# Kernel tuning notes

Measured on AMD Instinct MI355X. Metric: run time of the kernel, lower is better.

## Reference

```python
import jax, jax.numpy as jnp
import numpy as np

EMB = 512
HID = 1024
BATCH = 64
TX = 512


def setup_inputs() -> dict:
    key = jax.random.key(0)
    ks = jax.random.split(key, 9)
    s = 0.05
    return {
        "word": jax.random.normal(ks[0], (BATCH, TX, EMB), dtype=jnp.float32),
        "Wz": jax.random.normal(ks[1], (HID, HID + EMB), dtype=jnp.float32) * s,
        "bz": jax.random.normal(ks[2], (HID,), dtype=jnp.float32) * s,
        "Wr": jax.random.normal(ks[3], (HID, HID + EMB), dtype=jnp.float32) * s,
        "br": jax.random.normal(ks[4], (HID,), dtype=jnp.float32) * s,
        "Wh": jax.random.normal(ks[5], (HID, HID + EMB), dtype=jnp.float32) * s,
        "bh": jax.random.normal(ks[6], (HID,), dtype=jnp.float32) * s,
        "Wy": jax.random.normal(ks[7], (EMB, HID), dtype=jnp.float32) * s,
        "by": jax.random.normal(ks[8], (EMB,), dtype=jnp.float32) * s,
    }


def reference(word, Wz, bz, Wr, br, Wh, bh, Wy, by):
    batch = word.shape[0]
    word_t = jnp.transpose(word, (1, 0, 2))  # [T, B, E]
    h0 = jnp.zeros((batch, HID), dtype=word.dtype)
    x0 = jnp.zeros((batch, EMB), dtype=word.dtype)

    def step(carry, w_i):
        h, x = carry  # x is the PREVIOUS timestep's word (lags by one, as in the torch code)
        comb = jnp.concatenate([h, x], axis=1)  # [B, HID+EMB]
        z = jax.nn.sigmoid(comb @ Wz.T + bz)
        r = jax.nn.sigmoid(comb @ Wr.T + br)
        comb2 = jnp.concatenate([r * h, x], axis=1)
        h_tilde = jnp.tanh(comb2 @ Wh.T + bh)
        h_new = (1.0 - z) * h + z * h_tilde
        y = h_new @ Wy.T + by  # [B, E]
        return (h_new, w_i), y

    _, ys = jax.lax.scan(step, (h0, x0), word_t)  # ys: [T, B, E]
    return jnp.transpose(ys, (1, 0, 2))  # [B, T, E]
```

## Files before the change

### kernel.cpp

```cpp
#include <hip/hip_runtime.h>
#include <hip/hip_bf16.h>


#define EMB 512
#define HID 1024
#define BATCHN 64
#define TLEN 512
#define CAT 1536
#define GROUPS 4
#define GB 16
#define WPG 32
#define HX_LD 1024
#define ZL_LD 34
#define GPAD 8

typedef __attribute__((ext_vector_type(8))) short bf16x8;
typedef __attribute__((ext_vector_type(4))) short s16x4;
typedef __attribute__((ext_vector_type(4))) float f32x4;
typedef unsigned int u32;
typedef unsigned long long u64;
typedef unsigned short u16;

__device__ __forceinline__ float bf2f(u16 u) {
  union { float f; u32 i; } v; v.i = ((u32)u) << 16; return v.f;
}
__device__ __forceinline__ u16 f2bf(float f) {
  union { float f; u32 i; } v; v.f = f;
  u32 r = v.i + 0x7fffu + ((v.i >> 16) & 1u);
  return (u16)(r >> 16);
}

__device__ __forceinline__ u64 ld_dc(const u16* p) {
  return __hip_atomic_load((const u64*)p, __ATOMIC_RELAXED, __HIP_MEMORY_SCOPE_AGENT);
}
__device__ __forceinline__ void st_dc16(u16* p, u16 v) {
  __hip_atomic_store(p, v, __ATOMIC_RELAXED, __HIP_MEMORY_SCOPE_AGENT);
}

__global__ __launch_bounds__(256) void convert_gate_w(const float* __restrict__ W,
                                                      u16* __restrict__ Wh_,
                                                      u16* __restrict__ Wx_) {
  int i = blockIdx.x * 256 + threadIdx.x;
  if (i >= HID * CAT) return;
  int row = i / CAT, col = i - row * CAT;
  u16 v = f2bf(W[i]);
  if (col < HID) Wh_[row * HID + col] = v;
  else           Wx_[row * EMB + (col - HID)] = v;
}

__global__ __launch_bounds__(256) void convert_wy(const float* __restrict__ W, u16* __restrict__ Wy_) {
  int i = blockIdx.x * 256 + threadIdx.x;
  if (i < EMB * HID) Wy_[i] = f2bf(W[i]);
}

__global__ __launch_bounds__(256) void proj_kernel(const float* __restrict__ word,
                                                   const u16* __restrict__ Wx,
                                                   const float* __restrict__ bias,
                                                   u16* __restrict__ P) {
  __shared__ __align__(16) u16 As[64][64 + GPAD];
  __shared__ __align__(16) u16 Bs[64][64 + GPAD];
  const int tid = threadIdx.x;
  const int wid = tid >> 6, lane = tid & 63;
  const int m0 = blockIdx.x * 64, n0 = blockIdx.y * 64;
  const int mw = (wid >> 1) * 32, nw = (wid & 1) * 32;
  f32x4 acc[2][2] = {};
  for (int k0 = 0; k0 < EMB; k0 += 64) {
#pragma unroll
    for (int it = 0; it < 4; ++it) {
      int e = (it * 256 + tid) * 4;
      int row = e >> 6, col = e & 63;
      int R = m0 + row;
      float4 a = make_float4(0.f, 0.f, 0.f, 0.f);
      if ((R & (TLEN - 1)) != 0)
        a = *reinterpret_cast<const float4*>(&word[(u64)(R - 1) * EMB + k0 + col]);
      s16x4 vv;
      vv[0] = (short)f2bf(a.x); vv[1] = (short)f2bf(a.y);
      vv[2] = (short)f2bf(a.z); vv[3] = (short)f2bf(a.w);
      *reinterpret_cast<s16x4*>(&As[row][col]) = vv;
    }
#pragma unroll
    for (int it = 0; it < 2; ++it) {
      int e = (it * 256 + tid) * 8;
      int row = e >> 6, col = e & 63;
      *reinterpret_cast<bf16x8*>(&Bs[row][col]) =
          *reinterpret_cast<const bf16x8*>(&Wx[(u64)(n0 + row) * EMB + k0 + col]);
    }
    __syncthreads();
#pragma unroll
    for (int kk = 0; kk < 2; ++kk) {
      const int kb = kk * 32 + 8 * (lane >> 4);
#pragma unroll
      for (int i = 0; i < 2; ++i) {
        bf16x8 a = *reinterpret_cast<const bf16x8*>(&As[mw + i * 16 + (lane & 15)][kb]);
#pragma unroll
        for (int j = 0; j < 2; ++j) {
          bf16x8 b = *reinterpret_cast<const bf16x8*>(&Bs[nw + j * 16 + (lane & 15)][kb]);
          acc[i][j] = __builtin_amdgcn_mfma_f32_16x16x32_bf16(a, b, acc[i][j], 0, 0, 0);
        }
      }
    }
    __syncthreads();
  }
#pragma unroll
  for (int i = 0; i < 2; ++i)
#pragma unroll
    for (int j = 0; j < 2; ++j) {
      int col = n0 + nw + j * 16 + (lane & 15);
      float bv = bias[col];
#pragma unroll
      for (int q = 0; q < 4; ++q) {
        int row = m0 + mw + i * 16 + 4 * (lane >> 4) + q;
        P[(u64)row * HID + col] = f2bf(acc[i][j][q] + bv);
      }
    }
}

__global__ __launch_bounds__(256) void out_gemm(const u16* __restrict__ H,
                                                const u16* __restrict__ Wy,
                                                const float* __restrict__ by,
                                                float* __restrict__ out) {
  __shared__ __align__(16) u16 As[64][64 + GPAD];
  __shared__ __align__(16) u16 Bs[64][64 + GPAD];
  const int tid = threadIdx.x;
  const int wid = tid >> 6, lane = tid & 63;
  const int m0 = blockIdx.x * 64, n0 = blockIdx.y * 64;
  const int mw = (wid >> 1) * 32, nw = (wid & 1) * 32;
  f32x4 acc[2][2] = {};
  for (int k0 = 0; k0 < HID; k0 += 64) {
#pragma unroll
    for (int it = 0; it < 2; ++it) {
      int e = (it * 256 + tid) * 8;
      int row = e >> 6, col = e & 63;
      *reinterpret_cast<bf16x8*>(&As[row][col]) =
          *reinterpret_cast<const bf16x8*>(&H[(u64)(m0 + row) * HID + k0 + col]);
      *reinterpret_cast<bf16x8*>(&Bs[row][col]) =
          *reinterpret_cast<const bf16x8*>(&Wy[(u64)(n0 + row) * HID + k0 + col]);
    }
    __syncthreads();
#pragma unroll
    for (int kk = 0; kk < 2; ++kk) {
      const int kb = kk * 32 + 8 * (lane >> 4);
#pragma unroll
      for (int i = 0; i < 2; ++i) {
        bf16x8 a = *reinterpret_cast<const bf16x8*>(&As[mw + i * 16 + (lane & 15)][kb]);
#pragma unroll
        for (int j = 0; j < 2; ++j) {
          bf16x8 b = *reinterpret_cast<const bf16x8*>(&Bs[nw + j * 16 + (lane & 15)][kb]);
          acc[i][j] = __builtin_amdgcn_mfma_f32_16x16x32_bf16(a, b, acc[i][j], 0, 0, 0);
        }
      }
    }
    __syncthreads();
  }
#pragma unroll
  for (int i = 0; i < 2; ++i)
#pragma unroll
    for (int j = 0; j < 2; ++j) {
      int col = n0 + nw + j * 16 + (lane & 15);
      float bv = by[col];
#pragma unroll
      for (int q = 0; q < 4; ++q) {
        int row = m0 + mw + i * 16 + 4 * (lane >> 4) + q;
        out[(u64)row * EMB + col] = acc[i][j][q] + bv;
      }
    }
}

__device__ __forceinline__ void poll_flags(u32* gflags, u32 target) {
  if (threadIdx.x < 64) {
    u32* addr = &gflags[((int)threadIdx.x & (WPG - 1)) * 16];
    for (;;) {
      u32 v = __hip_atomic_load(addr, __ATOMIC_RELAXED, __HIP_MEMORY_SCOPE_AGENT);
      if (!__any((int)(v < target))) break;
    }
  }
}

__global__ __launch_bounds__(256, 1) void gru_persistent(
    const u16* __restrict__ Wzh, const u16* __restrict__ Wrh, const u16* __restrict__ Whh,
    const u16* __restrict__ Pz, const u16* __restrict__ Pr, u16* __restrict__ PhH,
    u16* __restrict__ rhbuf, u32* flags) {
  __shared__ __align__(16) u16 hx[16 * HX_LD];
  __shared__ __align__(16) u16 zL[16 * ZL_LD];
  __shared__ __align__(16) float RED[4 * 64 * 4];

  const int tid = threadIdx.x;
  const int wid = tid >> 6;
  const int lane = tid & 63;
  const int l15 = lane & 15;
  const int k4 = lane >> 4;
  const int g = blockIdx.x & (GROUPS - 1);
  const int w = blockIdx.x >> 2;
  const int b0 = g * GB;
  const int j = wid & 1;
  const int gate = wid >> 1;
  const int kh = wid >> 1;
  const int colA = 32 * w + 16 * j + l15;
  const u16* __restrict__ PA = gate ? Pr : Pz;
  u32* gflags = flags + g * (WPG * 16);

  const int sw = (l15 & 7) << 3;

  const int srow = tid >> 4;
  const int soff = (tid & 15) * 4;
  const int ssw = (srow & 7) << 3;

  bf16x8 wfA[32];
#pragma unroll
  for (int s = 0; s < 32; ++s)
    wfA[s] = *reinterpret_cast<const bf16x8*>(
        (gate ? Wrh : Wzh) + (u64)colA * HID + 32 * s + k4 * 8);
  bf16x8 wfB[16];
#pragma unroll
  for (int s = 0; s < 16; ++s)
    wfB[s] = *reinterpret_cast<const bf16x8*>(
        Whh + (u64)colA * HID + kh * 512 + 32 * s + k4 * 8);
#pragma unroll
  for (int s = 0; s < 32; ++s) asm volatile("" : "+v"(wfA[s]));
#pragma unroll
  for (int s = 0; s < 16; ++s) asm volatile("" : "+v"(wfB[s]));

  for (int e = tid; e < 16 * HX_LD / 2; e += 256) reinterpret_cast<u32*>(hx)[e] = 0u;
  __syncthreads();

  float pAc[4], pBc[4];
#pragma unroll
  for (int q = 0; q < 4; ++q) {
    int m = 4 * k4 + q;
    pAc[q] = bf2f(PA[((u64)(b0 + m) * TLEN) * HID + colA]);
    pBc[q] = bf2f(PhH[((u64)(b0 + m) * TLEN) * HID + colA]);
  }

  float hprev[4] = {0.f, 0.f, 0.f, 0.f};
  u32 ph = 0;

  for (int t = 0; t < TLEN; ++t) {
    if (t > 0) {
      const u16* src = PhH + ((u64)(b0 + srow) * TLEN + (t - 1)) * HID + soff;
      u64 tmp[16];
#pragma unroll
      for (int i = 0; i < 16; ++i) tmp[i] = ld_dc(src + i * 64);
      u16* dst = &hx[srow * HX_LD];
#pragma unroll
      for (int i = 0; i < 16; ++i)
        *reinterpret_cast<u64*>(dst + ((soff + i * 64) ^ ssw)) = tmp[i];
      __syncthreads();
    }

    f32x4 acc = {0.f, 0.f, 0.f, 0.f}, acc_b = {0.f, 0.f, 0.f, 0.f};
    if (t > 0) {
#pragma unroll
      for (int s = 0; s < 32; s += 2) {
        bf16x8 a0 = *reinterpret_cast<const bf16x8*>(
            &hx[l15 * HX_LD + ((32 * s + k4 * 8) ^ sw)]);
        bf16x8 a1 = *reinterpret_cast<const bf16x8*>(
            &hx[l15 * HX_LD + ((32 * (s + 1) + k4 * 8) ^ sw)]);
        acc   = __builtin_amdgcn_mfma_f32_16x16x32_bf16(a0, wfA[s],     acc,   0, 0, 0);
        acc_b = __builtin_amdgcn_mfma_f32_16x16x32_bf16(a1, wfA[s + 1], acc_b, 0, 0, 0);
      }
    }
#pragma unroll
    for (int q = 0; q < 4; ++q) {
      int m = 4 * k4 + q;
      float pre = acc[q] + acc_b[q] + pAc[q];
      float sg = 1.f / (1.f + __expf(-pre));
      if (gate == 0) {
        zL[m * ZL_LD + 16 * j + l15] = f2bf(sg);
      } else {
        st_dc16(rhbuf + (u64)(g * GB + m) * HID + colA, f2bf(sg * hprev[q]));
      }
    }

    ++ph;
    __syncthreads();
    asm volatile("" ::: "memory");
    if (tid == w)
      __hip_atomic_store(&gflags[w * 16], ph, __ATOMIC_RELAXED, __HIP_MEMORY_SCOPE_AGENT);
    {
      int tn = (t + 1 < TLEN) ? (t + 1) : t;
#pragma unroll
      for (int q = 0; q < 4; ++q) {
        int m = 4 * k4 + q;
        pAc[q] = bf2f(PA[((u64)(b0 + m) * TLEN + tn) * HID + colA]);
      }
    }
    poll_flags(gflags, ph);
    __syncthreads();
    asm volatile("" ::: "memory");

    {
      const u16* src = rhbuf + (u64)(g * GB + srow) * HID + soff;
      u64 tmp[16];
#pragma unroll
      for (int i = 0; i < 16; ++i) tmp[i] = ld_dc(src + i * 64);
      u16* dst = &hx[srow * HX_LD];
#pragma unroll
      for (int i = 0; i < 16; ++i)
        *reinterpret_cast<u64*>(dst + ((soff + i * 64) ^ ssw)) = tmp[i];
      __syncthreads();
    }

    f32x4 acc2 = {0.f, 0.f, 0.f, 0.f}, acc2b = {0.f, 0.f, 0.f, 0.f};
#pragma unroll
    for (int s = 0; s < 16; s += 2) {
      bf16x8 a0 = *reinterpret_cast<const bf16x8*>(
          &hx[l15 * HX_LD + ((kh * 512 + 32 * s + k4 * 8) ^ sw)]);
      bf16x8 a1 = *reinterpret_cast<const bf16x8*>(
          &hx[l15 * HX_LD + ((kh * 512 + 32 * (s + 1) + k4 * 8) ^ sw)]);
      acc2  = __builtin_amdgcn_mfma_f32_16x16x32_bf16(a0, wfB[s],     acc2,  0, 0, 0);
      acc2b = __builtin_amdgcn_mfma_f32_16x16x32_bf16(a1, wfB[s + 1], acc2b, 0, 0, 0);
    }
#pragma unroll
    for (int q = 0; q < 4; ++q) acc2[q] += acc2b[q];
    *reinterpret_cast<f32x4*>(&RED[(wid * 64 + lane) * 4]) = acc2;
    __syncthreads();
    {
      f32x4 part = *reinterpret_cast<const f32x4*>(&RED[((wid ^ 2) * 64 + lane) * 4]);
#pragma unroll
      for (int q = 0; q < 4; ++q) {
        int m = 4 * k4 + q;
        float pre = acc2[q] + part[q] + pBc[q];
        float e2 = __expf(2.f * pre);
        float th = 1.f - 2.f / (e2 + 1.f);
        float zq = bf2f(zL[m * ZL_LD + 16 * j + l15]);
        float hn = (1.f - zq) * hprev[q] + zq * th;
        hprev[q] = hn;
        if (wid < 2)
          st_dc16(PhH + ((u64)(b0 + m) * TLEN + t) * HID + colA, f2bf(hn));
      }
    }

    ++ph;
    __syncthreads();
    asm volatile("" ::: "memory");
    if (tid == w)
      __hip_atomic_store(&gflags[w * 16], ph, __ATOMIC_RELAXED, __HIP_MEMORY_SCOPE_AGENT);
    {
      int tn = (t + 1 < TLEN) ? (t + 1) : t;
#pragma unroll
      for (int q = 0; q < 4; ++q) {
        int m = 4 * k4 + q;
        pBc[q] = bf2f(PhH[((u64)(b0 + m) * TLEN + tn) * HID + colA]);
      }
    }
    poll_flags(gflags, ph);
    __syncthreads();
    asm volatile("" ::: "memory");
  }
}

extern "C" void kernel_launch(void* const* d_in, const int* in_sizes, int n_in,
                              void* d_out, int out_size, void* d_ws, size_t ws_size,
                              hipStream_t stream) {
  const float* word = (const float*)d_in[0];
  const float* Wz = (const float*)d_in[1];
  const float* bz = (const float*)d_in[2];
  const float* Wr = (const float*)d_in[3];
  const float* br = (const float*)d_in[4];
  const float* Wh = (const float*)d_in[5];
  const float* bh = (const float*)d_in[6];
  const float* Wy = (const float*)d_in[7];
  const float* by = (const float*)d_in[8];
  float* out = (float*)d_out;
  (void)in_sizes; (void)n_in; (void)out_size; (void)ws_size;

  char* ws = (char*)d_ws;
  size_t off = 0;
  auto alloc = [&](size_t bytes) {
    char* p = ws + off;
    off += (bytes + 255) & ~(size_t)255;
    return p;
  };
  u32* flags = (u32*)alloc(GROUPS * WPG * 16 * sizeof(u32));
  u16* WzhB = (u16*)alloc((size_t)HID * HID * 2);
  u16* WrhB = (u16*)alloc((size_t)HID * HID * 2);
  u16* WhhB = (u16*)alloc((size_t)HID * HID * 2);
  u16* WzxB = (u16*)alloc((size_t)HID * EMB * 2);
  u16* WrxB = (u16*)alloc((size_t)HID * EMB * 2);
  u16* WhxB = (u16*)alloc((size_t)HID * EMB * 2);
  u16* WyB  = (u16*)alloc((size_t)EMB * HID * 2);
  u16* Pr   = (u16*)alloc((size_t)BATCHN * TLEN * HID * 2);
  u16* PhH  = (u16*)alloc((size_t)BATCHN * TLEN * HID * 2);
  u16* rhbuf = (u16*)alloc((size_t)GROUPS * GB * HID * 2);
  u16* Pz = (u16*)d_out;

  hipMemsetAsync(flags, 0, GROUPS * WPG * 16 * sizeof(u32), stream);

  convert_gate_w<<<(HID * CAT + 255) / 256, 256, 0, stream>>>(Wz, WzhB, WzxB);
  convert_gate_w<<<(HID * CAT + 255) / 256, 256, 0, stream>>>(Wr, WrhB, WrxB);
  convert_gate_w<<<(HID * CAT + 255) / 256, 256, 0, stream>>>(Wh, WhhB, WhxB);
  convert_wy<<<(EMB * HID + 255) / 256, 256, 0, stream>>>(Wy, WyB);

  dim3 pg(512, 16);
  proj_kernel<<<pg, 256, 0, stream>>>(word, WzxB, bz, Pz);
  proj_kernel<<<pg, 256, 0, stream>>>(word, WrxB, br, Pr);
  proj_kernel<<<pg, 256, 0, stream>>>(word, WhxB, bh, PhH);

  gru_persistent<<<dim3(GROUPS * WPG), dim3(256), 0, stream>>>(WzhB, WrhB, WhhB, Pz, Pr, PhH,
                                                               rhbuf, flags);

  out_gemm<<<dim3(512, 8), 256, 0, stream>>>(PhH, WyB, by, out);
}
```

Baseline: 2.941 ms.

## Replace flag barriers with data-embedded parity tags and double-buffered exchange

Drops the per-workgroup flag stores and polling barriers between the gate phase and the candidate phase. Instead, each exchanged bf16 value carries a parity tag in its low mantissa bit, and consumers spin on the data itself in double-buffered rh and h buffers. This is meant to remove two global flag round-trips and two block syncs per timestep. In exchange it perturbs bf16 rounding by one ulp, relies on ordering of 64-bit relaxed loads, and has a retry cap that could silently accept stale data.

```diff
diff --git a/kernel.cpp b/kernel.cpp
--- a/kernel.cpp
+++ b/kernel.cpp
@@ -13,6 +13,7 @@
 #define HX_LD 1024
 #define ZL_LD 34
 #define GPAD 8
+#define RETRY_CAP 16384
 
 typedef __attribute__((ext_vector_type(8))) short bf16x8;
 typedef __attribute__((ext_vector_type(4))) short s16x4;
@@ -28,6 +29,17 @@
   union { float f; u32 i; } v; v.f = f;
   u32 r = v.i + 0x7fffu + ((v.i >> 16) & 1u);
   return (u16)(r >> 16);
+}
+__device__ __forceinline__ u16 f2bf_tag(float f, u32 tag) {
+  union { float f; u32 i; } v; v.f = f;
+  u32 r = v.i + 0x7fffu + ((v.i >> 16) & 1u);
+  u32 b = r >> 16;
+  if ((b ^ tag) & 1u) {
+    u32 dir = ((v.i >> 15) & 1u) ? 1u : (u32)-1;
+    if ((b & 0x7FFFu) == 0u) dir = 1u;
+    b += dir;
+  }
+  return (u16)b;
 }
 
 __device__ __forceinline__ u64 ld_dc(const u16* p) {
@@ -166,20 +178,10 @@
     }
 }
 
-__device__ __forceinline__ void poll_flags(u32* gflags, u32 target) {
-  if (threadIdx.x < 64) {
-    u32* addr = &gflags[((int)threadIdx.x & (WPG - 1)) * 16];
-    for (;;) {
-      u32 v = __hip_atomic_load(addr, __ATOMIC_RELAXED, __HIP_MEMORY_SCOPE_AGENT);
-      if (!__any((int)(v < target))) break;
-    }
-  }
-}
-
 __global__ __launch_bounds__(256, 1) void gru_persistent(
     const u16* __restrict__ Wzh, const u16* __restrict__ Wrh, const u16* __restrict__ Whh,
     const u16* __restrict__ Pz, const u16* __restrict__ Pr, u16* __restrict__ PhH,
-    u16* __restrict__ rhbuf, u32* flags) {
+    u16* __restrict__ rhbuf, u16* __restrict__ hxbuf) {
   __shared__ __align__(16) u16 hx[16 * HX_LD];
   __shared__ __align__(16) u16 zL[16 * ZL_LD];
   __shared__ __align__(16) float RED[4 * 64 * 4];
@@ -197,10 +199,9 @@
   const int kh = wid >> 1;
   const int colA = 32 * w + 16 * j + l15;
   const u16* __restrict__ PA = gate ? Pr : Pz;
-  u32* gflags = flags + g * (WPG * 16);
+  const u64 TM = 0x0001000100010001ull;
 
   const int sw = (l15 & 7) << 3;
-
   const int srow = tid >> 4;
   const int soff = (tid & 15) * 4;
   const int ssw = (srow & 7) << 3;
@@ -223,23 +224,37 @@
   for (int e = tid; e < 16 * HX_LD / 2; e += 256) reinterpret_cast<u32*>(hx)[e] = 0u;
   __syncthreads();
 
-  float pAc[4], pBc[4];
+  u16 pAr[4], pBr[4];
 #pragma unroll
   for (int q = 0; q < 4; ++q) {
     int m = 4 * k4 + q;
-    pAc[q] = bf2f(PA[((u64)(b0 + m) * TLEN) * HID + colA]);
-    pBc[q] = bf2f(PhH[((u64)(b0 + m) * TLEN) * HID + colA]);
+    pAr[q] = PA[((u64)(b0 + m) * TLEN) * HID + colA];
+    pBr[q] = PhH[((u64)(b0 + m) * TLEN) * HID + colA];
   }
 
   float hprev[4] = {0.f, 0.f, 0.f, 0.f};
-  u32 ph = 0;
 
   for (int t = 0; t < TLEN; ++t) {
+    const u32 tag = ((u32)t >> 1) & 1u;
+    const u64 base = (u64)(t & 1) * (BATCHN * HID);
+
     if (t > 0) {
-      const u16* src = PhH + ((u64)(b0 + srow) * TLEN + (t - 1)) * HID + soff;
+      const u32 etag = ((u32)(t - 1) >> 1) & 1u;
+      const u64 want = etag ? TM : 0ull;
+      const u16* src = hxbuf + (u64)((t - 1) & 1) * (BATCHN * HID) +
+                       (u64)(b0 + srow) * HID + soff;
       u64 tmp[16];
-#pragma unroll
-      for (int i = 0; i < 16; ++i) tmp[i] = ld_dc(src + i * 64);
+      u32 pend = 0xFFFFu;
+      int guard = 0;
+      while (pend && guard < RETRY_CAP) {
+#pragma unroll
+        for (int i = 0; i < 16; ++i)
+          if (pend & (1u << i)) tmp[i] = ld_dc(src + i * 64);
+#pragma unroll
+        for (int i = 0; i < 16; ++i)
+          if ((pend & (1u << i)) && ((tmp[i] & TM) == want)) pend &= ~(1u << i);
+        ++guard;
+      }
       u16* dst = &hx[srow * HX_LD];
 #pragma unroll
       for (int i = 0; i < 16; ++i)
@@ -262,37 +277,40 @@
 #pragma unroll
     for (int q = 0; q < 4; ++q) {
       int m = 4 * k4 + q;
-      float pre = acc[q] + acc_b[q] + pAc[q];
+      float pre = acc[q] + acc_b[q] + bf2f(pAr[q]);
       float sg = 1.f / (1.f + __expf(-pre));
       if (gate == 0) {
         zL[m * ZL_LD + 16 * j + l15] = f2bf(sg);
       } else {
-        st_dc16(rhbuf + (u64)(g * GB + m) * HID + colA, f2bf(sg * hprev[q]));
-      }
-    }
-
-    ++ph;
-    __syncthreads();
-    asm volatile("" ::: "memory");
-    if (tid == w)
-      __hip_atomic_store(&gflags[w * 16], ph, __ATOMIC_RELAXED, __HIP_MEMORY_SCOPE_AGENT);
+        st_dc16(rhbuf + base + (u64)(g * GB + m) * HID + colA,
+                f2bf_tag(sg * hprev[q], tag));
+      }
+    }
     {
       int tn = (t + 1 < TLEN) ? (t + 1) : t;
 #pragma unroll
       for (int q = 0; q < 4; ++q) {
         int m = 4 * k4 + q;
-        pAc[q] = bf2f(PA[((u64)(b0 + m) * TLEN + tn) * HID + colA]);
-      }
-    }
-    poll_flags(gflags, ph);
-    __syncthreads();
-    asm volatile("" ::: "memory");
+        pAr[q] = PA[((u64)(b0 + m) * TLEN + tn) * HID + colA];
+      }
+    }
+    __syncthreads();
 
     {
-      const u16* src = rhbuf + (u64)(g * GB + srow) * HID + soff;
+      const u64 want = tag ? TM : 0ull;
+      const u16* src = rhbuf + base + (u64)(g * GB + srow) * HID + soff;
       u64 tmp[16];
-#pragma unroll
-      for (int i = 0; i < 16; ++i) tmp[i] = ld_dc(src + i * 64);
+      u32 pend = 0xFFFFu;
+      int guard = 0;
+      while (pend && guard < RETRY_CAP) {
+#pragma unroll
+        for (int i = 0; i < 16; ++i)
+          if (pend & (1u << i)) tmp[i] = ld_dc(src + i * 64);
+#pragma unroll
+        for (int i = 0; i < 16; ++i)
+          if ((pend & (1u << i)) && ((tmp[i] & TM) == want)) pend &= ~(1u << i);
+        ++guard;
+      }
       u16* dst = &hx[srow * HX_LD];
 #pragma unroll
       for (int i = 0; i < 16; ++i)
@@ -319,33 +337,26 @@
 #pragma unroll
       for (int q = 0; q < 4; ++q) {
         int m = 4 * k4 + q;
-        float pre = acc2[q] + part[q] + pBc[q];
+        float pre = acc2[q] + part[q] + bf2f(pBr[q]);
         float e2 = __expf(2.f * pre);
         float th = 1.f - 2.f / (e2 + 1.f);
         float zq = bf2f(zL[m * ZL_LD + 16 * j + l15]);
         float hn = (1.f - zq) * hprev[q] + zq * th;
         hprev[q] = hn;
-        if (wid < 2)
-          st_dc16(PhH + ((u64)(b0 + m) * TLEN + t) * HID + colA, f2bf(hn));
-      }
-    }
-
-    ++ph;
-    __syncthreads();
-    asm volatile("" ::: "memory");
-    if (tid == w)
-      __hip_atomic_store(&gflags[w * 16], ph, __ATOMIC_RELAXED, __HIP_MEMORY_SCOPE_AGENT);
+        if (wid < 2) {
+          PhH[((u64)(b0 + m) * TLEN + t) * HID + colA] = f2bf(hn);
+          st_dc16(hxbuf + base + (u64)(b0 + m) * HID + colA, f2bf_tag(hn, tag));
+        }
+      }
+    }
     {
       int tn = (t + 1 < TLEN) ? (t + 1) : t;
 #pragma unroll
       for (int q = 0; q < 4; ++q) {
         int m = 4 * k4 + q;
-        pBc[q] = bf2f(PhH[((u64)(b0 + m) * TLEN + tn) * HID + colA]);
-      }
-    }
-    poll_flags(gflags, ph);
-    __syncthreads();
-    asm volatile("" ::: "memory");
+        pBr[q] = PhH[((u64)(b0 + m) * TLEN + tn) * HID + colA];
+      }
+    }
   }
 }
 
@@ -371,7 +382,8 @@
     off += (bytes + 255) & ~(size_t)255;
     return p;
   };
-  u32* flags = (u32*)alloc(GROUPS * WPG * 16 * sizeof(u32));
+  u16* rhbuf = (u16*)alloc((size_t)2 * BATCHN * HID * 2);
+  u16* hxbuf = (u16*)alloc((size_t)2 * BATCHN * HID * 2);
   u16* WzhB = (u16*)alloc((size_t)HID * HID * 2);
   u16* WrhB = (u16*)alloc((size_t)HID * HID * 2);
   u16* WhhB = (u16*)alloc((size_t)HID * HID * 2);
@@ -381,10 +393,9 @@
   u16* WyB  = (u16*)alloc((size_t)EMB * HID * 2);
   u16* Pr   = (u16*)alloc((size_t)BATCHN * TLEN * HID * 2);
   u16* PhH  = (u16*)alloc((size_t)BATCHN * TLEN * HID * 2);
-  u16* rhbuf = (u16*)alloc((size_t)GROUPS * GB * HID * 2);
   u16* Pz = (u16*)d_out;
 
-  hipMemsetAsync(flags, 0, GROUPS * WPG * 16 * sizeof(u32), stream);
+  hipMemsetAsync(rhbuf, 0xFF, (size_t)4 * BATCHN * HID * 2, stream);
 
   convert_gate_w<<<(HID * CAT + 255) / 256, 256, 0, stream>>>(Wz, WzhB, WzxB);
   convert_gate_w<<<(HID * CAT + 255) / 256, 256, 0, stream>>>(Wr, WrhB, WrxB);
@@ -397,7 +408,7 @@
   proj_kernel<<<pg, 256, 0, stream>>>(word, WhxB, bh, PhH);
 
   gru_persistent<<<dim3(GROUPS * WPG), dim3(256), 0, stream>>>(WzhB, WrhB, WhhB, Pz, Pr, PhH,
-                                                               rhbuf, flags);
+                                                               rhbuf, hxbuf);
 
   out_gemm<<<dim3(512, 8), 256, 0, stream>>>(PhH, WyB, by, out);
 }
```

Result: slower. 4.982 ms (+69.4%).

## Fuse three input projections into one kernel and poll flags from every wave

Applied to the files above, without the earlier changes.

The three separate projection GEMMs become a single kernel that loads and converts the word tile once and multiplies it against all three gate weight tiles, so the fp32 input is read and converted once instead of three times. In the persistent GRU loop, every wave now polls the group flags itself, which removes the __syncthreads that followed polling by wave 0 alone. The prefetched projection values are kept as bf16 in registers and converted when used, which lowers register pressure. The fused projection kernel uses more LDS and accumulators, and dropping the barrier depends on each wave's own polling to provide correct ordering.

```diff
diff --git a/kernel.cpp b/kernel.cpp
--- a/kernel.cpp
+++ b/kernel.cpp
@@ -53,17 +53,19 @@
   if (i < EMB * HID) Wy_[i] = f2bf(W[i]);
 }
 
-__global__ __launch_bounds__(256) void proj_kernel(const float* __restrict__ word,
-                                                   const u16* __restrict__ Wx,
-                                                   const float* __restrict__ bias,
-                                                   u16* __restrict__ P) {
+__global__ __launch_bounds__(256) void proj3_kernel(
+    const float* __restrict__ word,
+    const u16* __restrict__ Wzx, const u16* __restrict__ Wrx, const u16* __restrict__ Whx,
+    const float* __restrict__ bz, const float* __restrict__ br, const float* __restrict__ bh,
+    u16* __restrict__ Pz, u16* __restrict__ Pr, u16* __restrict__ Ph) {
   __shared__ __align__(16) u16 As[64][64 + GPAD];
-  __shared__ __align__(16) u16 Bs[64][64 + GPAD];
+  __shared__ __align__(16) u16 Bs[3][64][64 + GPAD];
   const int tid = threadIdx.x;
   const int wid = tid >> 6, lane = tid & 63;
   const int m0 = blockIdx.x * 64, n0 = blockIdx.y * 64;
   const int mw = (wid >> 1) * 32, nw = (wid & 1) * 32;
-  f32x4 acc[2][2] = {};
+  const u16* __restrict__ Wx[3] = {Wzx, Wrx, Whx};
+  f32x4 acc[3][2][2] = {};
   for (int k0 = 0; k0 < EMB; k0 += 64) {
 #pragma unroll
     for (int it = 0; it < 4; ++it) {
@@ -79,12 +81,14 @@
       *reinterpret_cast<s16x4*>(&As[row][col]) = vv;
     }
 #pragma unroll
-    for (int it = 0; it < 2; ++it) {
-      int e = (it * 256 + tid) * 8;
-      int row = e >> 6, col = e & 63;
-      *reinterpret_cast<bf16x8*>(&Bs[row][col]) =
-          *reinterpret_cast<const bf16x8*>(&Wx[(u64)(n0 + row) * EMB + k0 + col]);
-    }
+    for (int p = 0; p < 3; ++p)
+#pragma unroll
+      for (int it = 0; it < 2; ++it) {
+        int e = (it * 256 + tid) * 8;
+        int row = e >> 6, col = e & 63;
+        *reinterpret_cast<bf16x8*>(&Bs[p][row][col]) =
+            *reinterpret_cast<const bf16x8*>(&Wx[p][(u64)(n0 + row) * EMB + k0 + col]);
+      }
     __syncthreads();
 #pragma unroll
     for (int kk = 0; kk < 2; ++kk) {
@@ -93,26 +97,32 @@
       for (int i = 0; i < 2; ++i) {
         bf16x8 a = *reinterpret_cast<const bf16x8*>(&As[mw + i * 16 + (lane & 15)][kb]);
 #pragma unroll
-        for (int j = 0; j < 2; ++j) {
-          bf16x8 b = *reinterpret_cast<const bf16x8*>(&Bs[nw + j * 16 + (lane & 15)][kb]);
-          acc[i][j] = __builtin_amdgcn_mfma_f32_16x16x32_bf16(a, b, acc[i][j], 0, 0, 0);
+        for (int p = 0; p < 3; ++p)
+#pragma unroll
+          for (int j = 0; j < 2; ++j) {
+            bf16x8 b = *reinterpret_cast<const bf16x8*>(&Bs[p][nw + j * 16 + (lane & 15)][kb]);
+            acc[p][i][j] = __builtin_amdgcn_mfma_f32_16x16x32_bf16(a, b, acc[p][i][j], 0, 0, 0);
+          }
+      }
+    }
+    __syncthreads();
+  }
+  u16* __restrict__ Pout[3] = {Pz, Pr, Ph};
+  const float* __restrict__ bias[3] = {bz, br, bh};
+#pragma unroll
+  for (int p = 0; p < 3; ++p)
+#pragma unroll
+    for (int i = 0; i < 2; ++i)
+#pragma unroll
+      for (int j = 0; j < 2; ++j) {
+        int col = n0 + nw + j * 16 + (lane & 15);
+        float bv = bias[p][col];
+#pragma unroll
+        for (int q = 0; q < 4; ++q) {
+          int row = m0 + mw + i * 16 + 4 * (lane >> 4) + q;
+          Pout[p][(u64)row * HID + col] = f2bf(acc[p][i][j][q] + bv);
         }
       }
-    }
-    __syncthreads();
-  }
-#pragma unroll
-  for (int i = 0; i < 2; ++i)
-#pragma unroll
-    for (int j = 0; j < 2; ++j) {
-      int col = n0 + nw + j * 16 + (lane & 15);
-      float bv = bias[col];
-#pragma unroll
-      for (int q = 0; q < 4; ++q) {
-        int row = m0 + mw + i * 16 + 4 * (lane >> 4) + q;
-        P[(u64)row * HID + col] = f2bf(acc[i][j][q] + bv);
-      }
-    }
 }
 
 __global__ __launch_bounds__(256) void out_gemm(const u16* __restrict__ H,
@@ -166,13 +176,15 @@
     }
 }
 
-__device__ __forceinline__ void poll_flags(u32* gflags, u32 target) {
-  if (threadIdx.x < 64) {
-    u32* addr = &gflags[((int)threadIdx.x & (WPG - 1)) * 16];
-    for (;;) {
-      u32 v = __hip_atomic_load(addr, __ATOMIC_RELAXED, __HIP_MEMORY_SCOPE_AGENT);
-      if (!__any((int)(v < target))) break;
-    }
+__device__ __forceinline__ void poll_flags_wave(u32* gflags, u32 target) {
+  const int lane = threadIdx.x & 63;
+  const int active = (lane < WPG) ? 1 : 0;
+  u32* addr = &gflags[(lane & (WPG - 1)) * 16];
+  for (;;) {
+    u32 v = target;
+    if (active)
+      v = __hip_atomic_load(addr, __ATOMIC_RELAXED, __HIP_MEMORY_SCOPE_AGENT);
+    if (!__any((int)(v < target))) break;
   }
 }
 
@@ -200,7 +212,6 @@
   u32* gflags = flags + g * (WPG * 16);
 
   const int sw = (l15 & 7) << 3;
-
   const int srow = tid >> 4;
   const int soff = (tid & 15) * 4;
   const int ssw = (srow & 7) << 3;
@@ -223,12 +234,12 @@
   for (int e = tid; e < 16 * HX_LD / 2; e += 256) reinterpret_cast<u32*>(hx)[e] = 0u;
   __syncthreads();
 
-  float pAc[4], pBc[4];
+  u16 pAr[4], pBr[4];
 #pragma unroll
   for (int q = 0; q < 4; ++q) {
     int m = 4 * k4 + q;
-    pAc[q] = bf2f(PA[((u64)(b0 + m) * TLEN) * HID + colA]);
-    pBc[q] = bf2f(PhH[((u64)(b0 + m) * TLEN) * HID + colA]);
+    pAr[q] = PA[((u64)(b0 + m) * TLEN) * HID + colA];
+    pBr[q] = PhH[((u64)(b0 + m) * TLEN) * HID + colA];
   }
 
   float hprev[4] = {0.f, 0.f, 0.f, 0.f};
@@ -262,7 +273,7 @@
 #pragma unroll
     for (int q = 0; q < 4; ++q) {
       int m = 4 * k4 + q;
-      float pre = acc[q] + acc_b[q] + pAc[q];
+      float pre = acc[q] + acc_b[q] + bf2f(pAr[q]);
       float sg = 1.f / (1.f + __expf(-pre));
       if (gate == 0) {
         zL[m * ZL_LD + 16 * j + l15] = f2bf(sg);
@@ -281,11 +292,10 @@
 #pragma unroll
       for (int q = 0; q < 4; ++q) {
         int m = 4 * k4 + q;
-        pAc[q] = bf2f(PA[((u64)(b0 + m) * TLEN + tn) * HID + colA]);
-      }
-    }
-    poll_flags(gflags, ph);
-    __syncthreads();
+        pAr[q] = PA[((u64)(b0 + m) * TLEN + tn) * HID + colA];
+      }
+    }
+    poll_flags_wave(gflags, ph);
     asm volatile("" ::: "memory");
 
     {
@@ -319,7 +329,7 @@
 #pragma unroll
       for (int q = 0; q < 4; ++q) {
         int m = 4 * k4 + q;
-        float pre = acc2[q] + part[q] + pBc[q];
+        float pre = acc2[q] + part[q] + bf2f(pBr[q]);
         float e2 = __expf(2.f * pre);
         float th = 1.f - 2.f / (e2 + 1.f);
         float zq = bf2f(zL[m * ZL_LD + 16 * j + l15]);
@@ -340,11 +350,10 @@
 #pragma unroll
       for (int q = 0; q < 4; ++q) {
         int m = 4 * k4 + q;
-        pBc[q] = bf2f(PhH[((u64)(b0 + m) * TLEN + tn) * HID + colA]);
-      }
-    }
-    poll_flags(gflags, ph);
-    __syncthreads();
+        pBr[q] = PhH[((u64)(b0 + m) * TLEN + tn) * HID + colA];
+      }
+    }
+    poll_flags_wave(gflags, ph);
     asm volatile("" ::: "memory");
   }
 }
@@ -391,10 +400,8 @@
   convert_gate_w<<<(HID * CAT + 255) / 256, 256, 0, stream>>>(Wh, WhhB, WhxB);
   convert_wy<<<(EMB * HID + 255) / 256, 256, 0, stream>>>(Wy, WyB);
 
-  dim3 pg(512, 16);
-  proj_kernel<<<pg, 256, 0, stream>>>(word, WzxB, bz, Pz);
-  proj_kernel<<<pg, 256, 0, stream>>>(word, WrxB, br, Pr);
-  proj_kernel<<<pg, 256, 0, stream>>>(word, WhxB, bh, PhH);
+  proj3_kernel<<<dim3(512, 16), 256, 0, stream>>>(word, WzxB, WrxB, WhxB,
+                                                  bz, br, bh, Pz, Pr, PhH);
 
   gru_persistent<<<dim3(GROUPS * WPG), dim3(256), 0, stream>>>(WzhB, WrhB, WhhB, Pz, Pr, PhH,
                                                                rhbuf, flags);
```

Result: no change. 2.921 ms (-0.7%).
